# Performance work log

Hardware: AMD Instinct MI355X
Metric: run time of the kernel (lower is better)

The kernel has to match this reference:

```python
import jax, jax.numpy as jnp
import numpy as np

SEQ, D_MODEL, N_HEADS, D_INT = 2048, 1024, 16, 64
D_OUT = D_MODEL // N_HEADS  # 64


def setup_inputs() -> dict:
    key = jax.random.key(0)
    ks = jax.random.split(key, 9)
    s = lambda fan_in: 1.0 / np.sqrt(fan_in)
    return {
        "input_vecs": jax.random.normal(ks[0], (8, SEQ, D_MODEL), dtype=jnp.float32),
        # weights stored [in, out] (torch Linear weight transposed)
        "Wk": jax.random.uniform(ks[1], (D_MODEL, D_INT), minval=-s(D_MODEL), maxval=s(D_MODEL)),
        "bk": jax.random.uniform(ks[2], (D_INT,), minval=-s(D_MODEL), maxval=s(D_MODEL)),
        "Wq": jax.random.uniform(ks[3], (D_MODEL, D_INT), minval=-s(D_MODEL), maxval=s(D_MODEL)),
        "bq": jax.random.uniform(ks[4], (D_INT,), minval=-s(D_MODEL), maxval=s(D_MODEL)),
        "Wv": jax.random.uniform(ks[5], (D_MODEL, D_INT), minval=-s(D_MODEL), maxval=s(D_MODEL)),
        "bv": jax.random.uniform(ks[6], (D_INT,), minval=-s(D_MODEL), maxval=s(D_MODEL)),
        "W0": jax.random.uniform(ks[7], (D_INT, D_OUT), minval=-s(D_INT), maxval=s(D_INT)),
        "b0": jax.random.uniform(ks[8], (D_OUT,), minval=-s(D_INT), maxval=s(D_INT)),
    }


def reference(input_vecs, Wk, bk, Wq, bq, Wv, bv, W0, b0):
    # Projections: [B, T, d_int]
    k = jnp.einsum("btd,de->bte", input_vecs, Wk) + bk
    q = jnp.einsum("btd,de->bte", input_vecs, Wq) + bq
    v = jnp.einsum("btd,de->bte", input_vecs, Wv) + bv
    d_k = k.shape[-1]
    # Causal scores: [B, T, T]
    scores = jnp.einsum("bqe,bke->bqk", q, k) * (d_k ** -0.5)
    T = scores.shape[-1]
    causal = jnp.tril(jnp.ones((T, T), dtype=bool))
    scores = jnp.where(causal, scores, -jnp.inf)
    attn = jax.nn.softmax(scores, axis=-1)
    ctx = jnp.einsum("bqk,bke->bqe", attn, v)  # [B, T, d_int]
    return jnp.einsum("bte,eo->bto", ctx, W0) + b0  # [B, T, d_model//num_heads]
```

## Files before the change

kernel.cpp:

```cpp
#include <hip/hip_runtime.h>
#include <math.h>

#define SEQ 2048
#define DM  1024
#define DI  64

typedef __attribute__((ext_vector_type(8))) short short8;
typedef __attribute__((ext_vector_type(4))) float f32x4;
typedef __attribute__((ext_vector_type(4))) unsigned short ush4;

#define MFMA16(a,b,c) __builtin_amdgcn_mfma_f32_16x16x32_bf16(a,b,c,0,0,0)

__device__ __forceinline__ unsigned short f2bf(float f) {
    unsigned int u = __builtin_bit_cast(unsigned int, f);
    u += 0x7fffu + ((u >> 16) & 1u);
    return (unsigned short)(u >> 16);
}


__global__ __launch_bounds__(256)
void convert_kernel(const float* __restrict__ X,
                    const float* __restrict__ Wq, const float* __restrict__ Wk,
                    const float* __restrict__ Wv, const float* __restrict__ W0,
                    const float* __restrict__ bq, const float* __restrict__ bk,
                    const float* __restrict__ bv,
                    unsigned short* __restrict__ Wf, unsigned short* __restrict__ W0f,
                    unsigned short* __restrict__ Xf, float* __restrict__ bcat)
{
    const int t = threadIdx.x;
    const int blk = blockIdx.x;
    if (blk < 96) {
        const int flat = blk * 256 + t;
        const int lane = flat & 63;
        const int s    = (flat >> 6) & 1;
        const int gk   = flat >> 7;
        const int g = gk >> 4, ks = gk & 15;
        const int n = lane & 15, quad = lane >> 4;
        const int ocat = 16 * g + n;
        const int mat = ocat >> 6, o = ocat & 63;
        const float* src = (mat == 0) ? Wq : (mat == 1) ? Wk : Wv;
        const float scale = (mat == 0) ? 0.125f : 1.0f;
        const int kb = ks * 64 + s * 32 + quad * 8;
        union { short8 v; unsigned short u[8]; } pk;
#pragma unroll
        for (int e = 0; e < 8; ++e)
            pk.u[e] = f2bf(src[(size_t)(kb + e) * DI + o] * scale);
        *(short8*)(Wf + (size_t)flat * 8) = pk.v;
    } else if (blk < 98) {
        const int flat = (blk - 96) * 256 + t;
        if (flat < 512) {
            const int lane = flat & 63;
            const int s    = (flat >> 6) & 1;
            const int g    = flat >> 7;
            const int n = lane & 15, quad = lane >> 4;
            const int o = 16 * g + n;
            const int kb = s * 32 + quad * 8;
            union { short8 v; unsigned short u[8]; } pk;
#pragma unroll
            for (int e = 0; e < 8; ++e)
                pk.u[e] = f2bf(W0[(size_t)(kb + e) * DI + o]);
            *(short8*)(W0f + (size_t)flat * 8) = pk.v;
        }
        if (blk == 96 && t < 192)
            bcat[t] = (t < 64) ? bq[t] * 0.125f : (t < 128) ? bk[t - 64] : bv[t - 128];
    } else {
        const int gid = (blk - 98) * 256 + t;
        const int lane = gid & 63;
        const int s    = (gid >> 6) & 1;
        const int gk   = gid >> 7;
        const int g16 = gk >> 4, ks = gk & 15;
        const int n = lane & 15, quad = lane >> 4;
        const int row = g16 * 16 + n;
        const int k = ks * 64 + s * 32 + quad * 8;
        const float4 a = *(const float4*)(X + (size_t)row * DM + k);
        const float4 c = *(const float4*)(X + (size_t)row * DM + k + 4);
        union { short8 v; unsigned short u[8]; } pk;
        pk.u[0] = f2bf(a.x); pk.u[1] = f2bf(a.y); pk.u[2] = f2bf(a.z); pk.u[3] = f2bf(a.w);
        pk.u[4] = f2bf(c.x); pk.u[5] = f2bf(c.y); pk.u[6] = f2bf(c.z); pk.u[7] = f2bf(c.w);
        *(short8*)(Xf + (size_t)gid * 8) = pk.v;
    }
}

__global__ __launch_bounds__(256, 4)
void proj_kernel(const unsigned short* __restrict__ Xf, const unsigned short* __restrict__ Wf,
                 const float* __restrict__ bcat,
                 unsigned short* __restrict__ Qf, unsigned short* __restrict__ Kf,
                 unsigned short* __restrict__ Vf)
{
    __shared__ alignas(16) unsigned short Facc[16][200];
    const int t = threadIdx.x;
    const int lane = t & 63, w = t >> 6;
    const int quad = lane >> 4, n = lane & 15;
    const int g16 = blockIdx.x;
    const int r0 = g16 * 16;

    const unsigned short* abase = Xf + (size_t)g16 * 16384 + lane * 8;
    const unsigned short* wb0 = Wf + (size_t)(3 * w + 0) * 16384 + lane * 8;
    const unsigned short* wb1 = Wf + (size_t)(3 * w + 1) * 16384 + lane * 8;
    const unsigned short* wb2 = Wf + (size_t)(3 * w + 2) * 16384 + lane * 8;

    const f32x4 ZERO = {0.f, 0.f, 0.f, 0.f};
    f32x4 acc[3] = {ZERO, ZERO, ZERO};

#pragma unroll 4
    for (int ks = 0; ks < 16; ++ks) {
        short8 af[2], bf[3][2];
#pragma unroll
        for (int s = 0; s < 2; ++s) {
            const size_t o = (size_t)(ks * 2 + s) * 512;
            af[s]    = *(const short8*)(abase + o);
            bf[0][s] = *(const short8*)(wb0 + o);
            bf[1][s] = *(const short8*)(wb1 + o);
            bf[2][s] = *(const short8*)(wb2 + o);
        }
#pragma unroll
        for (int j = 0; j < 3; ++j) {
            acc[j] = MFMA16(af[0], bf[j][0], acc[j]);
            acc[j] = MFMA16(af[1], bf[j][1], acc[j]);
        }
    }

#pragma unroll
    for (int j = 0; j < 3; ++j) {
        const float bias = bcat[(3 * w + j) * 16 + n];
#pragma unroll
        for (int r = 0; r < 4; ++r)
            Facc[quad * 4 + r][(3 * w + j) * 16 + n] = f2bf(acc[j][r] + bias);
    }
    __syncthreads();

    const int bidx = r0 >> 11;
    const int qt16 = (r0 >> 4) & 127;
    const int kc   = (r0 >> 6) & 31;
    const int sblk = (r0 >> 5) & 1;
    if (t < 128) {
        const int s = t >> 6, lp = t & 63;
        const int np = lp & 15, qp = lp >> 4;
        const size_t off = (size_t)(((bidx * 128 + qt16) * 2 + s) * 64 + lp) * 8;
        *(short8*)(Qf + off) = *(const short8*)&Facc[np][s * 32 + qp * 8];
        *(short8*)(Kf + off) = *(const short8*)&Facc[np][64 + s * 32 + qp * 8];
    } else {
        const int i = t - 128;
        const int nt = i >> 5, lp = i & 31;
        const int q2 = (r0 & 31) >> 3;
        const int quadp = q2 + (lp >> 4), np = lp & 15;
        const int lanep = quadp * 16 + np;
        union { short8 v; unsigned short u[8]; } ov;
#pragma unroll
        for (int e = 0; e < 8; ++e) ov.u[e] = Facc[(lp >> 4) * 8 + e][128 + 16 * nt + np];
        const size_t off = (size_t)((((bidx * 4 + nt) * 32 + kc) * 2 + sblk) * 64 + lanep) * 8;
        *(short8*)(Vf + off) = ov.v;
    }
}

__global__ __launch_bounds__(256, 3)
void attn_kernel(const unsigned short* __restrict__ Qf, const unsigned short* __restrict__ Kf,
                 const unsigned short* __restrict__ Vf, const unsigned short* __restrict__ W0f,
                 const float* __restrict__ b0, float* __restrict__ Out)
{
    __shared__ alignas(16) float pool[4][32][72];
    __shared__ alignas(16) unsigned short Cb[32][72];
    __shared__ float Lp[4][32][4];

    const int t = threadIdx.x;
    const int lane = t & 63, w = t >> 6;
    const int quad = lane >> 4, n = lane & 15;
    const int qt = 63 - (blockIdx.x >> 3);
    const int b  = blockIdx.x & 7;
    const int q0 = qt * 32;

    unsigned short* P = (unsigned short*)&pool[w][0][0];

    short8 qf[2][2];
#pragma unroll
    for (int qh = 0; qh < 2; ++qh)
#pragma unroll
        for (int s = 0; s < 2; ++s)
            qf[qh][s] = *(const short8*)(Qf + (size_t)(((b*128 + qt*2 + qh)*2 + s)*64 + lane) * 8);

    const f32x4 ZERO = {0.f, 0.f, 0.f, 0.f};
    f32x4 ctx[2][4];
#pragma unroll
    for (int qh = 0; qh < 2; ++qh)
#pragma unroll
        for (int nt = 0; nt < 4; ++nt) ctx[qh][nt] = ZERO;
    float rs[2] = {0.f, 0.f};
    const float M0 = 8.0f;

    const int C = (qt >> 1) + 1;
    for (int kt = w; kt < C; kt += 4) {
        const int k0 = kt * 64;
        short8 kf[4][2];
#pragma unroll
        for (int tt = 0; tt < 4; ++tt)
#pragma unroll
            for (int s = 0; s < 2; ++s)
                kf[tt][s] = *(const short8*)(Kf + (size_t)(((b*128 + kt*4 + tt)*2 + s)*64 + lane) * 8);
        f32x4 sv[2][4];
#pragma unroll
        for (int qh = 0; qh < 2; ++qh)
#pragma unroll
            for (int tt = 0; tt < 4; ++tt) {
                f32x4 a = MFMA16(kf[tt][0], qf[qh][0], ZERO);
                sv[qh][tt] = MFMA16(kf[tt][1], qf[qh][1], a);
            }
        short8 vf[4][2];
#pragma unroll
        for (int nt = 0; nt < 4; ++nt)
#pragma unroll
            for (int s = 0; s < 2; ++s)
                vf[nt][s] = *(const short8*)(Vf + (size_t)((((b*4 + nt)*32 + kt)*2 + s)*64 + lane) * 8);
        if (kt == C - 1) {
#pragma unroll
            for (int qh = 0; qh < 2; ++qh)
#pragma unroll
                for (int tt = 0; tt < 4; ++tt)
#pragma unroll
                    for (int r = 0; r < 4; ++r)
                        if (k0 + 16*tt + quad*4 + r > q0 + qh*16 + n)
                            sv[qh][tt][r] = -INFINITY;
        }
#pragma unroll
        for (int qh = 0; qh < 2; ++qh)
#pragma unroll
            for (int tt = 0; tt < 4; ++tt) {
                union { ush4 v; unsigned short u[4]; } pw;
#pragma unroll
                for (int r = 0; r < 4; ++r) {
                    const float p = __expf(sv[qh][tt][r] - M0);
                    rs[qh] += p;
                    pw.u[r] = f2bf(p);
                }
                *(ush4*)&P[(size_t)(qh*16 + n) * 72 + 16*tt + quad*4] = pw.v;
            }
#pragma unroll
        for (int s = 0; s < 2; ++s) {
            const short8 pf0 = *(const short8*)&P[(size_t)(n)      * 72 + s*32 + quad*8];
            const short8 pf1 = *(const short8*)&P[(size_t)(16 + n) * 72 + s*32 + quad*8];
#pragma unroll
            for (int nt = 0; nt < 4; ++nt) {
                ctx[0][nt] = MFMA16(pf0, vf[nt][s], ctx[0][nt]);
                ctx[1][nt] = MFMA16(pf1, vf[nt][s], ctx[1][nt]);
            }
        }
    }
#pragma unroll
    for (int qh = 0; qh < 2; ++qh) {
#pragma unroll
        for (int nt = 0; nt < 4; ++nt)
#pragma unroll
            for (int r = 0; r < 4; ++r)
                pool[w][qh*16 + quad*4 + r][nt*16 + n] = ctx[qh][nt][r];
        Lp[w][qh*16 + n][quad] = rs[qh];
    }
    __syncthreads();

    {
        const int q = t >> 3, c0 = (t & 7) * 8;
        float l = 0.f;
#pragma unroll
        for (int w4 = 0; w4 < 4; ++w4)
#pragma unroll
            for (int qd = 0; qd < 4; ++qd) l += Lp[w4][q][qd];
        const float inv = 1.0f / l;
        float s[8];
#pragma unroll
        for (int j = 0; j < 8; ++j) s[j] = 0.f;
#pragma unroll
        for (int w4 = 0; w4 < 4; ++w4) {
            const float4 a = *(const float4*)&pool[w4][q][c0];
            const float4 c = *(const float4*)&pool[w4][q][c0 + 4];
            s[0] += a.x; s[1] += a.y; s[2] += a.z; s[3] += a.w;
            s[4] += c.x; s[5] += c.y; s[6] += c.z; s[7] += c.w;
        }
        union { short8 v; unsigned short u[8]; } cb;
#pragma unroll
        for (int j = 0; j < 8; ++j) cb.u[j] = f2bf(s[j] * inv);
        *(short8*)&Cb[q][c0] = cb.v;
    }
    __syncthreads();

    f32x4 oacc[2] = {ZERO, ZERO};
#pragma unroll
    for (int s = 0; s < 2; ++s) {
        const short8 wf = *(const short8*)(W0f + (size_t)((w*2 + s)*64 + lane) * 8);
#pragma unroll
        for (int tt = 0; tt < 2; ++tt) {
            const short8 cf = *(const short8*)&Cb[tt*16 + n][s*32 + quad*8];
            oacc[tt] = MFMA16(cf, wf, oacc[tt]);
        }
    }
    const float bb = b0[16*w + n];
#pragma unroll
    for (int tt = 0; tt < 2; ++tt)
#pragma unroll
        for (int r = 0; r < 4; ++r)
            Out[((size_t)b * SEQ + q0 + tt*16 + quad*4 + r) * DI + 16*w + n] = oacc[tt][r] + bb;
}

extern "C" void kernel_launch(void* const* d_in, const int* in_sizes, int n_in,
                              void* d_out, int out_size, void* d_ws, size_t ws_size,
                              hipStream_t stream) {
    const float* X  = (const float*)d_in[0];
    const float* Wk = (const float*)d_in[1];
    const float* bk = (const float*)d_in[2];
    const float* Wq = (const float*)d_in[3];
    const float* bq = (const float*)d_in[4];
    const float* Wv = (const float*)d_in[5];
    const float* bv = (const float*)d_in[6];
    const float* W0 = (const float*)d_in[7];
    const float* b0 = (const float*)d_in[8];
    float* Out = (float*)d_out;

    unsigned char* ws = (unsigned char*)d_ws;
    unsigned short* Wf   = (unsigned short*)ws;
    unsigned short* W0f  = (unsigned short*)(ws + 393216);
    float*          bcat = (float*)(ws + 401408);
    unsigned short* Qf   = (unsigned short*)(ws + 409600);
    unsigned short* Kf   = (unsigned short*)(ws + 409600 + 2097152);
    unsigned short* Vf   = (unsigned short*)(ws + 409600 + 4194304);
    unsigned short* Xf   = (unsigned short*)(ws + 8388608);

    convert_kernel<<<8290, 256, 0, stream>>>(X, Wq, Wk, Wv, W0, bq, bk, bv,
                                             Wf, W0f, Xf, bcat);
    proj_kernel<<<1024, 256, 0, stream>>>(Xf, Wf, bcat, Qf, Kf, Vf);
    attn_kernel<<<512, 256, 0, stream>>>(Qf, Kf, Vf, W0f, b0, Out);
}
```

Baseline: 142.2 us.

## Fuse X fp32-to-bf16 conversion into projection kernel via LDS staging

The projection kernel now reads fp32 activations directly, converts them to bf16, and stores them in shared memory in MFMA fragment order. This replaces the separate conversion pass that wrote a bf16 copy of X to global memory and read it back. The convert kernel now only handles the weights and shrinks to 98 blocks. In exchange the projection kernel needs 32KB of LDS, which may lower occupancy, and it adds a sync before the GEMM loop.

```diff
diff --git a/kernel.cpp b/kernel.cpp
--- a/kernel.cpp
+++ b/kernel.cpp
@@ -19,13 +19,12 @@
 
 
 __global__ __launch_bounds__(256)
-void convert_kernel(const float* __restrict__ X,
-                    const float* __restrict__ Wq, const float* __restrict__ Wk,
+void convert_kernel(const float* __restrict__ Wq, const float* __restrict__ Wk,
                     const float* __restrict__ Wv, const float* __restrict__ W0,
                     const float* __restrict__ bq, const float* __restrict__ bk,
                     const float* __restrict__ bv,
                     unsigned short* __restrict__ Wf, unsigned short* __restrict__ W0f,
-                    unsigned short* __restrict__ Xf, float* __restrict__ bcat)
+                    float* __restrict__ bcat)
 {
     const int t = threadIdx.x;
     const int blk = blockIdx.x;
@@ -46,7 +45,7 @@
         for (int e = 0; e < 8; ++e)
             pk.u[e] = f2bf(src[(size_t)(kb + e) * DI + o] * scale);
         *(short8*)(Wf + (size_t)flat * 8) = pk.v;
-    } else if (blk < 98) {
+    } else {
         const int flat = (blk - 96) * 256 + t;
         if (flat < 512) {
             const int lane = flat & 63;
@@ -63,41 +62,42 @@
         }
         if (blk == 96 && t < 192)
             bcat[t] = (t < 64) ? bq[t] * 0.125f : (t < 128) ? bk[t - 64] : bv[t - 128];
-    } else {
-        const int gid = (blk - 98) * 256 + t;
-        const int lane = gid & 63;
-        const int s    = (gid >> 6) & 1;
-        const int gk   = gid >> 7;
-        const int g16 = gk >> 4, ks = gk & 15;
-        const int n = lane & 15, quad = lane >> 4;
-        const int row = g16 * 16 + n;
-        const int k = ks * 64 + s * 32 + quad * 8;
-        const float4 a = *(const float4*)(X + (size_t)row * DM + k);
-        const float4 c = *(const float4*)(X + (size_t)row * DM + k + 4);
-        union { short8 v; unsigned short u[8]; } pk;
-        pk.u[0] = f2bf(a.x); pk.u[1] = f2bf(a.y); pk.u[2] = f2bf(a.z); pk.u[3] = f2bf(a.w);
-        pk.u[4] = f2bf(c.x); pk.u[5] = f2bf(c.y); pk.u[6] = f2bf(c.z); pk.u[7] = f2bf(c.w);
-        *(short8*)(Xf + (size_t)gid * 8) = pk.v;
     }
 }
 
 __global__ __launch_bounds__(256, 4)
-void proj_kernel(const unsigned short* __restrict__ Xf, const unsigned short* __restrict__ Wf,
+void proj_kernel(const float* __restrict__ X, const unsigned short* __restrict__ Wf,
                  const float* __restrict__ bcat,
                  unsigned short* __restrict__ Qf, unsigned short* __restrict__ Kf,
                  unsigned short* __restrict__ Vf)
 {
-    __shared__ alignas(16) unsigned short Facc[16][200];
+    __shared__ alignas(16) unsigned short Xs[16 * 1024];
     const int t = threadIdx.x;
     const int lane = t & 63, w = t >> 6;
     const int quad = lane >> 4, n = lane & 15;
     const int g16 = blockIdx.x;
     const int r0 = g16 * 16;
 
-    const unsigned short* abase = Xf + (size_t)g16 * 16384 + lane * 8;
+    {
+        const int r = t >> 4, g = t & 15;
+        const float* xp = X + (size_t)(r0 + r) * DM + g * 4;
+        const int s = g >> 3, qd = (g >> 1) & 3, e0 = (g & 1) * 4;
+        const int base = (r * 4 + qd) * 8 + e0;
+#pragma unroll
+        for (int i = 0; i < 16; ++i) {
+            const float4 x = *(const float4*)(xp + i * 64);
+            union { ush4 v; unsigned short u[4]; } px;
+            px.u[0] = f2bf(x.x); px.u[1] = f2bf(x.y);
+            px.u[2] = f2bf(x.z); px.u[3] = f2bf(x.w);
+            *(ush4*)(Xs + (i * 2 + s) * 512 + base) = px.v;
+        }
+    }
+    __syncthreads();
+
     const unsigned short* wb0 = Wf + (size_t)(3 * w + 0) * 16384 + lane * 8;
     const unsigned short* wb1 = Wf + (size_t)(3 * w + 1) * 16384 + lane * 8;
     const unsigned short* wb2 = Wf + (size_t)(3 * w + 2) * 16384 + lane * 8;
+    const int aperm = (n * 4 + quad) * 8;
 
     const f32x4 ZERO = {0.f, 0.f, 0.f, 0.f};
     f32x4 acc[3] = {ZERO, ZERO, ZERO};
@@ -108,7 +108,7 @@
 #pragma unroll
         for (int s = 0; s < 2; ++s) {
             const size_t o = (size_t)(ks * 2 + s) * 512;
-            af[s]    = *(const short8*)(abase + o);
+            af[s]    = *(const short8*)(Xs + o + aperm);
             bf[0][s] = *(const short8*)(wb0 + o);
             bf[1][s] = *(const short8*)(wb1 + o);
             bf[2][s] = *(const short8*)(wb2 + o);
@@ -120,6 +120,8 @@
         }
     }
 
+    __syncthreads();
+    unsigned short (*Facc)[200] = (unsigned short (*)[200])Xs;
 #pragma unroll
     for (int j = 0; j < 3; ++j) {
         const float bias = bcat[(3 * w + j) * 16 + n];
@@ -319,10 +321,8 @@
     unsigned short* Qf   = (unsigned short*)(ws + 409600);
     unsigned short* Kf   = (unsigned short*)(ws + 409600 + 2097152);
     unsigned short* Vf   = (unsigned short*)(ws + 409600 + 4194304);
-    unsigned short* Xf   = (unsigned short*)(ws + 8388608);
-
-    convert_kernel<<<8290, 256, 0, stream>>>(X, Wq, Wk, Wv, W0, bq, bk, bv,
-                                             Wf, W0f, Xf, bcat);
-    proj_kernel<<<1024, 256, 0, stream>>>(Xf, Wf, bcat, Qf, Kf, Vf);
+
+    convert_kernel<<<98, 256, 0, stream>>>(Wq, Wk, Wv, W0, bq, bk, bv, Wf, W0f, bcat);
+    proj_kernel<<<1024, 256, 0, stream>>>(X, Wf, bcat, Qf, Kf, Vf);
     attn_kernel<<<512, 256, 0, stream>>>(Qf, Kf, Vf, W0f, b0, Out);
 }
```

Measured after the change: 132.8 us. 1.07x faster.
